# Kernel optimization log

Measured on AMD Instinct MI355X. Metric: run time of the kernel, lower is better.

The kernel has to match this reference:

```python
import jax, jax.numpy as jnp
import numpy as np

N = 8192
IN_FEATURES = 512
OUT_FEATURES = 256
ALPHA = 0.2  # leaky relu negative slope
NEG_PAD = jnp.float32(-2.0 ** 31)


def setup_inputs() -> dict:
    key = jax.random.key(0)
    k_h, k_adj, k_W, k_a = jax.random.split(key, 4)
    h = jax.random.normal(k_h, (N, IN_FEATURES), dtype=jnp.float32)
    adj = jax.random.randint(k_adj, (N, N), 0, 2, dtype=jnp.int32)
    # xavier_uniform with gain=1.414
    gain = 1.414
    lim_W = gain * np.sqrt(6.0 / (IN_FEATURES + OUT_FEATURES))
    W = jax.random.uniform(k_W, (IN_FEATURES, OUT_FEATURES), dtype=jnp.float32,
                           minval=-lim_W, maxval=lim_W)
    lim_a = gain * np.sqrt(6.0 / (2 * OUT_FEATURES + 1))
    a = jax.random.uniform(k_a, (2 * OUT_FEATURES, 1), dtype=jnp.float32,
                           minval=-lim_a, maxval=lim_a)
    return {"h": h, "adj": adj, "W": W, "a": a}


def reference(h, adj, W, a):
    # h: (N, F_in), adj: (N, N) int, W: (F_in, F_out), a: (2*F_out, 1)
    out_f = W.shape[1]
    Wh = h @ W                      # (N, F_out)
    Wh1 = Wh @ a[:out_f]            # (N, 1)  source scores
    Wh2 = Wh @ a[out_f:]            # (N, 1)  destination scores
    e = jax.nn.leaky_relu(Wh1 + Wh2.T, negative_slope=ALPHA)  # (N, N)
    masked = jnp.where(adj > 0, e, NEG_PAD)
    attention = jax.nn.softmax(masked, axis=1)
    # dropout is identity in eval mode (training=False)
    return attention
```

## Files before the change

kernel.cpp:

```cpp
#include <hip/hip_runtime.h>

#define N 8192
#define FIN 512
#define FOUT 256
#define ALPHA 0.2f
#define NEG_PAD (-2147483648.0f)

__global__ void gat_compute_u(const float* __restrict__ W,
                              const float* __restrict__ a,
                              float* __restrict__ u1,
                              float* __restrict__ u2) {
    int k = blockIdx.x * blockDim.x + threadIdx.x;
    if (k >= FIN) return;
    const float* wr = W + (size_t)k * FOUT;
    float acc1 = 0.f, acc2 = 0.f;
    #pragma unroll 4
    for (int f = 0; f < FOUT; ++f) {
        float w = wr[f];
        acc1 += w * a[f];
        acc2 += w * a[FOUT + f];
    }
    u1[k] = acc1;
    u2[k] = acc2;
}

__global__ __launch_bounds__(256) void gat_scores(const float* __restrict__ h,
                                                  const float* __restrict__ u1,
                                                  const float* __restrict__ u2,
                                                  float* __restrict__ s1,
                                                  float* __restrict__ s2) {
    int gtid = blockIdx.x * blockDim.x + threadIdx.x;
    int row  = gtid >> 6;
    int lane = gtid & 63;
    if (row >= N) return;
    const float* hr = h + (size_t)row * FIN;
    float a1 = 0.f, a2 = 0.f;
    #pragma unroll
    for (int it = 0; it < FIN / 256; ++it) {
        int base = it * 256 + lane * 4;
        float4 hv  = *(const float4*)(hr + base);
        float4 v1  = *(const float4*)(u1 + base);
        float4 v2  = *(const float4*)(u2 + base);
        a1 += hv.x * v1.x + hv.y * v1.y + hv.z * v1.z + hv.w * v1.w;
        a2 += hv.x * v2.x + hv.y * v2.y + hv.z * v2.z + hv.w * v2.w;
    }
    #pragma unroll
    for (int off = 32; off > 0; off >>= 1) {
        a1 += __shfl_xor(a1, off);
        a2 += __shfl_xor(a2, off);
    }
    if (lane == 0) {
        s1[row] = a1;
        s2[row] = a2;
    }
}

__global__ __launch_bounds__(256) void gat_attn_row(const int* __restrict__ adj,
                                                    const float* __restrict__ s1,
                                                    const float* __restrict__ s2,
                                                    float* __restrict__ out) {
    const int row = blockIdx.x;
    const int t   = threadIdx.x;

    const int4*   arow = (const int4*)(adj + (size_t)row * N);
    const float4* s2v  = (const float4*)s2;
    const float   s1i  = s1[row];

    float vals[32];
    float lmax = NEG_PAD;

    #pragma unroll
    for (int c = 0; c < 8; ++c) {
        int idx = c * 256 + t;
        int4   av = arow[idx];
        float4 sv = s2v[idx];
        float e0 = s1i + sv.x; e0 = (e0 > 0.f) ? e0 : ALPHA * e0; e0 = (av.x > 0) ? e0 : NEG_PAD;
        float e1 = s1i + sv.y; e1 = (e1 > 0.f) ? e1 : ALPHA * e1; e1 = (av.y > 0) ? e1 : NEG_PAD;
        float e2 = s1i + sv.z; e2 = (e2 > 0.f) ? e2 : ALPHA * e2; e2 = (av.z > 0) ? e2 : NEG_PAD;
        float e3 = s1i + sv.w; e3 = (e3 > 0.f) ? e3 : ALPHA * e3; e3 = (av.w > 0) ? e3 : NEG_PAD;
        vals[c * 4 + 0] = e0;
        vals[c * 4 + 1] = e1;
        vals[c * 4 + 2] = e2;
        vals[c * 4 + 3] = e3;
        lmax = fmaxf(lmax, fmaxf(fmaxf(e0, e1), fmaxf(e2, e3)));
    }

    __shared__ float red[8];
    #pragma unroll
    for (int off = 32; off > 0; off >>= 1)
        lmax = fmaxf(lmax, __shfl_xor(lmax, off));
    int wid = t >> 6;
    if ((t & 63) == 0) red[wid] = lmax;
    __syncthreads();
    float bmax = fmaxf(fmaxf(red[0], red[1]), fmaxf(red[2], red[3]));

    float lsum = 0.f;
    #pragma unroll
    for (int q = 0; q < 32; ++q) {
        float ev = __expf(vals[q] - bmax);
        vals[q] = ev;
        lsum += ev;
    }

    #pragma unroll
    for (int off = 32; off > 0; off >>= 1)
        lsum += __shfl_xor(lsum, off);
    if ((t & 63) == 0) red[4 + wid] = lsum;
    __syncthreads();
    float bsum = (red[4] + red[5]) + (red[6] + red[7]);
    float inv  = 1.0f / bsum;

    float4* orow = (float4*)(out + (size_t)row * N);
    #pragma unroll
    for (int c = 0; c < 8; ++c) {
        int idx = c * 256 + t;
        float4 o;
        o.x = vals[c * 4 + 0] * inv;
        o.y = vals[c * 4 + 1] * inv;
        o.z = vals[c * 4 + 2] * inv;
        o.w = vals[c * 4 + 3] * inv;
        orow[idx] = o;
    }
}

extern "C" void kernel_launch(void* const* d_in, const int* in_sizes, int n_in,
                              void* d_out, int out_size, void* d_ws, size_t ws_size,
                              hipStream_t stream) {
    const float* h   = (const float*)d_in[0];
    const int*   adj = (const int*)d_in[1];
    const float* W   = (const float*)d_in[2];
    const float* a   = (const float*)d_in[3];
    float*       out = (float*)d_out;

    float* u1 = (float*)d_ws;
    float* u2 = u1 + FIN;
    float* s1 = u2 + FIN;
    float* s2 = s1 + N;

    gat_compute_u<<<(FIN + 255) / 256, 256, 0, stream>>>(W, a, u1, u2);
    gat_scores<<<(N * 64) / 256, 256, 0, stream>>>(h, u1, u2, s1, s2);
    gat_attn_row<<<N, 256, 0, stream>>>(adj, s1, s2, out);
}
```

Before: 121.0 us.

## Use global s2 max as softmax shift to drop row max pass

A small kernel computes the global maximum of the destination scores. Because leaky ReLU is monotone, leaky_relu(s1_i + max s2) bounds every entry in row i, so the attention kernel uses it as the softmax shift. That removes the per-row max reduction and one block barrier, and exponentials are computed in the first pass. The adjacency loads and output stores become nontemporal and the block grows to 512 threads. The cost is underflow risk when a row's true masked max sits far below the bound, and a fully masked row now yields NaN instead of a uniform row.

```diff
diff --git a/kernel.cpp b/kernel.cpp
--- a/kernel.cpp
+++ b/kernel.cpp
@@ -4,7 +4,9 @@
 #define FIN 512
 #define FOUT 256
 #define ALPHA 0.2f
-#define NEG_PAD (-2147483648.0f)
+
+typedef int   iv4 __attribute__((ext_vector_type(4)));
+typedef float fv4 __attribute__((ext_vector_type(4)));
 
 __global__ void gat_compute_u(const float* __restrict__ W,
                               const float* __restrict__ a,
@@ -38,9 +40,9 @@
     #pragma unroll
     for (int it = 0; it < FIN / 256; ++it) {
         int base = it * 256 + lane * 4;
-        float4 hv  = *(const float4*)(hr + base);
-        float4 v1  = *(const float4*)(u1 + base);
-        float4 v2  = *(const float4*)(u2 + base);
+        fv4 hv  = *(const fv4*)(hr + base);
+        fv4 v1  = *(const fv4*)(u1 + base);
+        fv4 v2  = *(const fv4*)(u2 + base);
         a1 += hv.x * v1.x + hv.y * v1.y + hv.z * v1.z + hv.w * v1.w;
         a2 += hv.x * v2.x + hv.y * v2.y + hv.z * v2.z + hv.w * v2.w;
     }
@@ -55,71 +57,81 @@
     }
 }
 
-__global__ __launch_bounds__(256) void gat_attn_row(const int* __restrict__ adj,
+__global__ __launch_bounds__(256) void gat_s2max(const float* __restrict__ s2,
+                                                 float* __restrict__ s2max) {
+    int t = threadIdx.x;
+    float m = -3.0e38f;
+    for (int i = t; i < N; i += 256)
+        m = fmaxf(m, s2[i]);
+    #pragma unroll
+    for (int off = 32; off > 0; off >>= 1)
+        m = fmaxf(m, __shfl_xor(m, off));
+    __shared__ float red[4];
+    if ((t & 63) == 0) red[t >> 6] = m;
+    __syncthreads();
+    if (t == 0)
+        s2max[0] = fmaxf(fmaxf(red[0], red[1]), fmaxf(red[2], red[3]));
+}
+
+__global__ __launch_bounds__(512) void gat_attn_row(const int* __restrict__ adj,
                                                     const float* __restrict__ s1,
                                                     const float* __restrict__ s2,
+                                                    const float* __restrict__ s2max,
                                                     float* __restrict__ out) {
     const int row = blockIdx.x;
     const int t   = threadIdx.x;
 
-    const int4*   arow = (const int4*)(adj + (size_t)row * N);
-    const float4* s2v  = (const float4*)s2;
-    const float   s1i  = s1[row];
+    const float s1i = s1[row];
+    float M = s1i + s2max[0];
+    M = (M > 0.f) ? M : ALPHA * M;
 
-    float vals[32];
-    float lmax = NEG_PAD;
+    const iv4* arow = (const iv4*)(adj + (size_t)row * N);
+    const fv4* s2v  = (const fv4*)s2;
+
+    float p[16];
+    float lsum = 0.f;
 
     #pragma unroll
-    for (int c = 0; c < 8; ++c) {
-        int idx = c * 256 + t;
-        int4   av = arow[idx];
-        float4 sv = s2v[idx];
-        float e0 = s1i + sv.x; e0 = (e0 > 0.f) ? e0 : ALPHA * e0; e0 = (av.x > 0) ? e0 : NEG_PAD;
-        float e1 = s1i + sv.y; e1 = (e1 > 0.f) ? e1 : ALPHA * e1; e1 = (av.y > 0) ? e1 : NEG_PAD;
-        float e2 = s1i + sv.z; e2 = (e2 > 0.f) ? e2 : ALPHA * e2; e2 = (av.z > 0) ? e2 : NEG_PAD;
-        float e3 = s1i + sv.w; e3 = (e3 > 0.f) ? e3 : ALPHA * e3; e3 = (av.w > 0) ? e3 : NEG_PAD;
-        vals[c * 4 + 0] = e0;
-        vals[c * 4 + 1] = e1;
-        vals[c * 4 + 2] = e2;
-        vals[c * 4 + 3] = e3;
-        lmax = fmaxf(lmax, fmaxf(fmaxf(e0, e1), fmaxf(e2, e3)));
-    }
-
-    __shared__ float red[8];
-    #pragma unroll
-    for (int off = 32; off > 0; off >>= 1)
-        lmax = fmaxf(lmax, __shfl_xor(lmax, off));
-    int wid = t >> 6;
-    if ((t & 63) == 0) red[wid] = lmax;
-    __syncthreads();
-    float bmax = fmaxf(fmaxf(red[0], red[1]), fmaxf(red[2], red[3]));
-
-    float lsum = 0.f;
-    #pragma unroll
-    for (int q = 0; q < 32; ++q) {
-        float ev = __expf(vals[q] - bmax);
-        vals[q] = ev;
-        lsum += ev;
+    for (int c = 0; c < 4; ++c) {
+        int idx = c * 512 + t;
+        iv4 av = __builtin_nontemporal_load(arow + idx);
+        fv4 sv = s2v[idx];
+        float e0 = s1i + sv.x; e0 = (e0 > 0.f) ? e0 : ALPHA * e0;
+        float e1 = s1i + sv.y; e1 = (e1 > 0.f) ? e1 : ALPHA * e1;
+        float e2 = s1i + sv.z; e2 = (e2 > 0.f) ? e2 : ALPHA * e2;
+        float e3 = s1i + sv.w; e3 = (e3 > 0.f) ? e3 : ALPHA * e3;
+        float p0 = (av.x > 0) ? __expf(e0 - M) : 0.f;
+        float p1 = (av.y > 0) ? __expf(e1 - M) : 0.f;
+        float p2 = (av.z > 0) ? __expf(e2 - M) : 0.f;
+        float p3 = (av.w > 0) ? __expf(e3 - M) : 0.f;
+        p[c * 4 + 0] = p0;
+        p[c * 4 + 1] = p1;
+        p[c * 4 + 2] = p2;
+        p[c * 4 + 3] = p3;
+        lsum += (p0 + p1) + (p2 + p3);
     }
 
     #pragma unroll
     for (int off = 32; off > 0; off >>= 1)
         lsum += __shfl_xor(lsum, off);
-    if ((t & 63) == 0) red[4 + wid] = lsum;
+    __shared__ float red[8];
+    int wid = t >> 6;
+    if ((t & 63) == 0) red[wid] = lsum;
     __syncthreads();
-    float bsum = (red[4] + red[5]) + (red[6] + red[7]);
-    float inv  = 1.0f / bsum;
+    float bsum = ((red[0] + red[1]) + (red[2] + red[3])) +
+                 ((red[4] + red[5]) + (red[6] + red[7]));
+    float inv = 1.0f / bsum;
 
-    float4* orow = (float4*)(out + (size_t)row * N);
+    fv4* orow = (fv4*)(out + (size_t)row * N);
     #pragma unroll
-    for (int c = 0; c < 8; ++c) {
-        int idx = c * 256 + t;
-        float4 o;
-        o.x = vals[c * 4 + 0] * inv;
-        o.y = vals[c * 4 + 1] * inv;
-        o.z = vals[c * 4 + 2] * inv;
-        o.w = vals[c * 4 + 3] * inv;
-        orow[idx] = o;
+    for (int c = 0; c < 4; ++c) {
+        int idx = c * 512 + t;
+        fv4 o;
+        o.x = p[c * 4 + 0] * inv;
+        o.y = p[c * 4 + 1] * inv;
+        o.z = p[c * 4 + 2] * inv;
+        o.w = p[c * 4 + 3] * inv;
+        __builtin_nontemporal_store(o, orow + idx);
     }
 }
 
@@ -132,12 +144,14 @@
     const float* a   = (const float*)d_in[3];
     float*       out = (float*)d_out;
 
-    float* u1 = (float*)d_ws;
-    float* u2 = u1 + FIN;
-    float* s1 = u2 + FIN;
-    float* s2 = s1 + N;
+    float* u1    = (float*)d_ws;
+    float* u2    = u1 + FIN;
+    float* s1    = u2 + FIN;
+    float* s2    = s1 + N;
+    float* s2max = s2 + N;
 
     gat_compute_u<<<(FIN + 255) / 256, 256, 0, stream>>>(W, a, u1, u2);
     gat_scores<<<(N * 64) / 256, 256, 0, stream>>>(h, u1, u2, s1, s2);
-    gat_attn_row<<<N, 256, 0, stream>>>(adj, s1, s2, out);
+    gat_s2max<<<1, 256, 0, stream>>>(s2, s2max);
+    gat_attn_row<<<N, 512, 0, stream>>>(adj, s1, s2, s2max, out);
 }
```

Result: faster. 113.3 us (-6.4%).
